# Kernel tuning notes

Hardware: AMD Instinct MI355X
Metric: run time of the kernel (lower is better)

Reference implementation:

```python
import jax, jax.numpy as jnp
import numpy as np

NUM_CLASSES = 12
C_SMOOTH = 5.0  # the `c` constant in compute_weights(distances, 5)


def setup_inputs() -> dict:
    key = jax.random.key(0)
    k1, k2 = jax.random.split(key)
    features = jax.random.normal(k1, (128, 512, 32, 32), dtype=jnp.float32)
    labels = jax.random.randint(k2, (128,), 0, NUM_CLASSES)
    return {"features": features, "labels": labels}


def _prototype_generation(features, labels, num_classes):
    # features: [b, c, h, w]; labels: [b] int
    b = features.shape[0]
    flat = features.reshape(b, -1)  # [b, d], d = c*h*w
    sq = jnp.sum(flat * flat, axis=1)  # [b]
    d2 = sq[:, None] + sq[None, :] - 2.0 * (flat @ flat.T)  # [b, b]
    d2 = jnp.maximum(d2, 0.0)
    # grad-safe sqrt: diagonal (and identical pairs) get dist 0 with grad 0,
    # matching torch.norm's subgradient at 0
    pos = d2 > 0
    dist = jnp.where(pos, jnp.sqrt(jnp.where(pos, d2, 1.0)), 0.0)  # [b, b]
    # sum of distances to same-label samples (includes self, dist 0)
    same = (labels[:, None] == labels[None, :]).astype(flat.dtype)  # [b, b]
    dsum = jnp.sum(dist * same, axis=1)  # [b]
    # compute_weights(distance_sum, 5) = 1 / (sqrt(ds^2 + 25) + 1e-12)
    w = 1.0 / (jnp.sqrt(dsum * dsum + C_SMOOTH * C_SMOOTH) + 1e-12)
    w = w / (jnp.sum(w) + 1e-12)  # normalized sample weights [b]
    # label-grouped weighted scatter-sum -> [num_classes, c, h, w]
    weighted = features * w[:, None, None, None]
    return jax.ops.segment_sum(weighted, labels, num_segments=num_classes)


def reference(features, labels):
    return _prototype_generation(features, labels, NUM_CLASSES)
```

## Files before the change

### kernel.cpp

```cpp
#include <hip/hip_runtime.h>
#include <math.h>

#define D_FEAT 524288
#define NSAMP  128
#define NCLS   12
#define BK     256
#define KPB    2048
#define NB     256
#define D4     131072

typedef __bf16 bf16x8 __attribute__((ext_vector_type(8)));
typedef float  f32x16 __attribute__((ext_vector_type(16)));

__device__ __forceinline__ unsigned pack_bf16(float a, float b) {
  unsigned ua = __float_as_uint(a); ua += 0x7fffu + ((ua >> 16) & 1u);
  unsigned ub = __float_as_uint(b); ub += 0x7fffu + ((ub >> 16) & 1u);
  return (ua >> 16) | (ub & 0xffff0000u);
}

__global__ __launch_bounds__(512, 2) void gram_k(const float* __restrict__ f,
                                                 float* __restrict__ gram,
                                                 float* __restrict__ partial,
                                                 int atomic_mode) {
  __shared__ __align__(16) unsigned char lds[BK * NSAMP * 2];
  const int t    = threadIdx.x;
  const int b    = blockIdx.x;
  const int wave = t >> 6;
  const int lane = t & 63;
  const int sl   = lane & 31;
  const int hi   = lane >> 5;
  const int Ra   = (wave >> 2) * 64;
  const int Ca   = (wave & 3) * 32;
  const int kq   = lane;
  const size_t k0 = (size_t)b * KPB;

  f32x16 acc0, acc1;
#pragma unroll
  for (int i = 0; i < 16; ++i) { acc0[i] = 0.f; acc1[i] = 0.f; }

  const int wg      = kq >> 1;
  const int halfsel = kq & 1;

  float4 pf[16];
#pragma unroll
  for (int i = 0; i < 16; ++i) {
    const int s = i * 8 + wave;
    pf[i] = *(const float4*)(f + (size_t)s * D_FEAT + k0 + kq * 4);
  }
#pragma unroll
  for (int i = 0; i < 16; ++i) {
    const int s = i * 8 + wave;
    uint2 p; p.x = pack_bf16(pf[i].x, pf[i].y); p.y = pack_bf16(pf[i].z, pf[i].w);
    *(uint2*)(lds + (size_t)(wg * NSAMP + (s ^ (wg & 7))) * 16 + halfsel * 8) = p;
  }

  for (int sli = 0; sli < KPB / BK; ++sli) {
    __syncthreads();
    if (sli < KPB / BK - 1) {
      const size_t kb = k0 + (size_t)(sli + 1) * BK;
#pragma unroll
      for (int i = 0; i < 16; ++i) {
        const int s = i * 8 + wave;
        pf[i] = *(const float4*)(f + (size_t)s * D_FEAT + kb + kq * 4);
      }
    }
#pragma unroll
    for (int t16 = 0; t16 < 16; ++t16) {
      const int g = 2 * t16 + hi, gx = g & 7;
      const unsigned char* base = lds + g * (NSAMP * 16);
      bf16x8 a0 = *(const bf16x8*)(base + (((Ra      + sl) ^ gx) << 4));
      bf16x8 a1 = *(const bf16x8*)(base + (((Ra + 32 + sl) ^ gx) << 4));
      bf16x8 b0 = *(const bf16x8*)(base + (((Ca      + sl) ^ gx) << 4));
      acc0 = __builtin_amdgcn_mfma_f32_32x32x16_bf16(a0, b0, acc0, 0, 0, 0);
      acc1 = __builtin_amdgcn_mfma_f32_32x32x16_bf16(a1, b0, acc1, 0, 0, 0);
    }
    __syncthreads();
    if (sli < KPB / BK - 1) {
#pragma unroll
      for (int i = 0; i < 16; ++i) {
        const int s = i * 8 + wave;
        uint2 p; p.x = pack_bf16(pf[i].x, pf[i].y); p.y = pack_bf16(pf[i].z, pf[i].w);
        *(uint2*)(lds + (size_t)(wg * NSAMP + (s ^ (wg & 7))) * 16 + halfsel * 8) = p;
      }
    }
  }

  if (atomic_mode) {
#pragma unroll
    for (int r = 0; r < 16; ++r) {
      const int row0 = Ra + 4 * hi + (r & 3) + 8 * (r >> 2);
      atomicAdd(gram + row0 * NSAMP + Ca + sl, acc0[r]);
      atomicAdd(gram + (row0 + 32) * NSAMP + Ca + sl, acc1[r]);
    }
  } else {
    float* p = partial + (size_t)b * (NSAMP * NSAMP);
#pragma unroll
    for (int r = 0; r < 16; ++r) {
      const int row0 = Ra + 4 * hi + (r & 3) + 8 * (r >> 2);
      p[row0 * NSAMP + Ca + sl]        = acc0[r];
      p[(row0 + 32) * NSAMP + Ca + sl] = acc1[r];
    }
  }
}

__global__ __launch_bounds__(256) void reduce_k(const float* __restrict__ partial,
                                                float* __restrict__ gram) {
  const int idx = blockIdx.x * 256 + threadIdx.x;
  float s = 0.f;
#pragma unroll 8
  for (int b = 0; b < NB; ++b) s += partial[(size_t)b * (NSAMP * NSAMP) + idx];
  gram[idx] = s;
}

__global__ void weights_k(const float* __restrict__ gram, const int* __restrict__ labels,
                          float* __restrict__ w_out, int* __restrict__ order_out,
                          int* __restrict__ off_out) {
  __shared__ float sq[NSAMP];
  __shared__ int   lab[NSAMP];
  __shared__ float wv[NSAMP];
  __shared__ float wsum_s;
  __shared__ int   cnt[NCLS];
  __shared__ int   off[NCLS + 1];
  const int t = threadIdx.x;
  lab[t] = labels[t];
  sq[t]  = gram[t * NSAMP + t];
  if (t < NCLS) cnt[t] = 0;
  __syncthreads();
  const int   myl = lab[t];
  const float st  = sq[t];
  float dsum = 0.f;
  for (int j = 0; j < NSAMP; ++j) {
    if (j != t && lab[j] == myl) {
      float d2 = st + sq[j] - 2.f * gram[t * NSAMP + j];
      if (d2 > 0.f) dsum += sqrtf(d2);
    }
  }
  const float wt = 1.f / (sqrtf(dsum * dsum + 25.f) + 1e-12f);
  wv[t] = wt;
  atomicAdd(&cnt[myl], 1);
  __syncthreads();
  if (t == 0) {
    float s = 0.f;
    for (int j = 0; j < NSAMP; ++j) s += wv[j];
    wsum_s = s;
    off[0] = 0;
    for (int c = 0; c < NCLS; ++c) off[c + 1] = off[c] + cnt[c];
  }
  __syncthreads();
  int rank = 0;
  for (int j = 0; j < t; ++j) rank += (lab[j] == myl) ? 1 : 0;
  const int pos  = off[myl] + rank;
  order_out[pos] = t;
  w_out[pos]     = wt / (wsum_s + 1e-12f);
  if (t <= NCLS) off_out[t] = off[t];
}

__global__ __launch_bounds__(256) void scatter_k(const float* __restrict__ f,
                                                 const float* __restrict__ w,
                                                 const int* __restrict__ order,
                                                 const int* __restrict__ off,
                                                 float* __restrict__ out) {
  __shared__ float w_l[NSAMP];
  __shared__ int   ord_l[NSAMP];
  __shared__ int   off_l[NCLS + 1];
  const int t = threadIdx.x;
  if (t < NSAMP) { w_l[t] = w[t]; ord_l[t] = order[t]; }
  if (t <= NCLS) off_l[t] = off[t];
  __syncthreads();
  const size_t d4 = (size_t)blockIdx.x * 256 + t;
  const float4* f4 = (const float4*)f;
  float4* o4 = (float4*)out;
  for (int c = 0; c < NCLS; ++c) {
    float4 acc = make_float4(0.f, 0.f, 0.f, 0.f);
    const int e = off_l[c + 1];
#pragma unroll 4
    for (int j = off_l[c]; j < e; ++j) {
      const float  wj = w_l[j];
      const float4 v  = f4[(size_t)ord_l[j] * D4 + d4];
      acc.x += wj * v.x; acc.y += wj * v.y; acc.z += wj * v.z; acc.w += wj * v.w;
    }
    o4[(size_t)c * D4 + d4] = acc;
  }
}

extern "C" void kernel_launch(void* const* d_in, const int* in_sizes, int n_in,
                              void* d_out, int out_size, void* d_ws, size_t ws_size,
                              hipStream_t stream) {
  const float* f      = (const float*)d_in[0];
  const int*   labels = (const int*)d_in[1];
  float* out  = (float*)d_out;
  float* ws_f = (float*)d_ws;

  float* gram     = ws_f;
  float* w_sorted = ws_f + 16384;
  int*   order    = (int*)(ws_f + 16384 + 128);
  int*   clsoff   = (int*)(ws_f + 16384 + 256);
  float* partial  = ws_f + 32768;

  const size_t need = (size_t)32768 * 4 + (size_t)NB * NSAMP * NSAMP * 4;
  const int atomic_mode = (ws_size < need) ? 1 : 0;

  if (atomic_mode) hipMemsetAsync(gram, 0, NSAMP * NSAMP * sizeof(float), stream);
  gram_k<<<NB, 512, 0, stream>>>(f, gram, partial, atomic_mode);
  if (!atomic_mode) reduce_k<<<64, 256, 0, stream>>>(partial, gram);
  weights_k<<<1, NSAMP, 0, stream>>>(gram, labels, w_sorted, order, clsoff);
  scatter_k<<<D4 / 256, 256, 0, stream>>>(f, w_sorted, order, clsoff, out);
}
```

Measured before the change: 483.9 us.

## Double-buffer gram LDS tiles, widen reduce grid, stage gram in LDS for weights

The gram kernel now keeps two LDS buffers, so the next bf16 slice is written while the current one is read, and one barrier per iteration is dropped. The partial-sum reduce uses 256 blocks of 64 threads so more CUs pull data. The weights kernel copies the full gram matrix into LDS with 256 threads and sums the weights with a wave shuffle instead of a serial loop. LDS use in gram_k doubles to 128KB, which may limit the intended two blocks per CU.

Measured after the change: 473.0 us. 1.02x faster.

```diff
diff --git a/kernel.cpp b/kernel.cpp
--- a/kernel.cpp
+++ b/kernel.cpp
@@ -22,7 +22,7 @@
                                                  float* __restrict__ gram,
                                                  float* __restrict__ partial,
                                                  int atomic_mode) {
-  __shared__ __align__(16) unsigned char lds[BK * NSAMP * 2];
+  __shared__ __align__(16) unsigned char lds[2 * BK * NSAMP * 2];
   const int t    = threadIdx.x;
   const int b    = blockIdx.x;
   const int wave = t >> 6;
@@ -51,11 +51,13 @@
   for (int i = 0; i < 16; ++i) {
     const int s = i * 8 + wave;
     uint2 p; p.x = pack_bf16(pf[i].x, pf[i].y); p.y = pack_bf16(pf[i].z, pf[i].w);
-    *(uint2*)(lds + (size_t)(wg * NSAMP + (s ^ (wg & 7))) * 16 + halfsel * 8) = p;
+    *(uint2*)(lds + (wg * NSAMP + (s ^ (wg & 7))) * 16 + halfsel * 8) = p;
   }
 
   for (int sli = 0; sli < KPB / BK; ++sli) {
     __syncthreads();
+    const unsigned char* rb = lds + (sli & 1) * (BK * NSAMP * 2);
+    unsigned char*       wb = lds + ((sli + 1) & 1) * (BK * NSAMP * 2);
     if (sli < KPB / BK - 1) {
       const size_t kb = k0 + (size_t)(sli + 1) * BK;
 #pragma unroll
@@ -67,20 +69,19 @@
 #pragma unroll
     for (int t16 = 0; t16 < 16; ++t16) {
       const int g = 2 * t16 + hi, gx = g & 7;
-      const unsigned char* base = lds + g * (NSAMP * 16);
+      const unsigned char* base = rb + g * (NSAMP * 16);
       bf16x8 a0 = *(const bf16x8*)(base + (((Ra      + sl) ^ gx) << 4));
       bf16x8 a1 = *(const bf16x8*)(base + (((Ra + 32 + sl) ^ gx) << 4));
       bf16x8 b0 = *(const bf16x8*)(base + (((Ca      + sl) ^ gx) << 4));
       acc0 = __builtin_amdgcn_mfma_f32_32x32x16_bf16(a0, b0, acc0, 0, 0, 0);
       acc1 = __builtin_amdgcn_mfma_f32_32x32x16_bf16(a1, b0, acc1, 0, 0, 0);
     }
-    __syncthreads();
     if (sli < KPB / BK - 1) {
 #pragma unroll
       for (int i = 0; i < 16; ++i) {
         const int s = i * 8 + wave;
         uint2 p; p.x = pack_bf16(pf[i].x, pf[i].y); p.y = pack_bf16(pf[i].z, pf[i].w);
-        *(uint2*)(lds + (size_t)(wg * NSAMP + (s ^ (wg & 7))) * 16 + halfsel * 8) = p;
+        *(uint2*)(wb + (wg * NSAMP + (s ^ (wg & 7))) * 16 + halfsel * 8) = p;
       }
     }
   }
@@ -103,55 +104,72 @@
   }
 }
 
-__global__ __launch_bounds__(256) void reduce_k(const float* __restrict__ partial,
-                                                float* __restrict__ gram) {
-  const int idx = blockIdx.x * 256 + threadIdx.x;
+__global__ __launch_bounds__(64) void reduce_k(const float* __restrict__ partial,
+                                               float* __restrict__ gram) {
+  const int idx = blockIdx.x * 64 + threadIdx.x;
   float s = 0.f;
-#pragma unroll 8
+#pragma unroll 16
   for (int b = 0; b < NB; ++b) s += partial[(size_t)b * (NSAMP * NSAMP) + idx];
   gram[idx] = s;
 }
 
-__global__ void weights_k(const float* __restrict__ gram, const int* __restrict__ labels,
+__global__ __launch_bounds__(256) void weights_k(const float* __restrict__ gram,
+                          const int* __restrict__ labels,
                           float* __restrict__ w_out, int* __restrict__ order_out,
                           int* __restrict__ off_out) {
-  __shared__ float sq[NSAMP];
+  __shared__ __align__(16) float g[NSAMP * NSAMP];
   __shared__ int   lab[NSAMP];
   __shared__ float wv[NSAMP];
   __shared__ float wsum_s;
   __shared__ int   cnt[NCLS];
   __shared__ int   off[NCLS + 1];
   const int t = threadIdx.x;
-  lab[t] = labels[t];
-  sq[t]  = gram[t * NSAMP + t];
-  if (t < NCLS) cnt[t] = 0;
-  __syncthreads();
-  const int   myl = lab[t];
-  const float st  = sq[t];
-  float dsum = 0.f;
-  for (int j = 0; j < NSAMP; ++j) {
-    if (j != t && lab[j] == myl) {
-      float d2 = st + sq[j] - 2.f * gram[t * NSAMP + j];
-      if (d2 > 0.f) dsum += sqrtf(d2);
-    }
-  }
-  const float wt = 1.f / (sqrtf(dsum * dsum + 25.f) + 1e-12f);
-  wv[t] = wt;
-  atomicAdd(&cnt[myl], 1);
-  __syncthreads();
-  if (t == 0) {
-    float s = 0.f;
-    for (int j = 0; j < NSAMP; ++j) s += wv[j];
-    wsum_s = s;
-    off[0] = 0;
-    for (int c = 0; c < NCLS; ++c) off[c + 1] = off[c] + cnt[c];
-  }
-  __syncthreads();
-  int rank = 0;
-  for (int j = 0; j < t; ++j) rank += (lab[j] == myl) ? 1 : 0;
-  const int pos  = off[myl] + rank;
-  order_out[pos] = t;
-  w_out[pos]     = wt / (wsum_s + 1e-12f);
+
+  {
+    float4* g4 = (float4*)g;
+    const float4* s4 = (const float4*)gram;
+#pragma unroll
+    for (int i = 0; i < 16; ++i) g4[i * 256 + t] = s4[i * 256 + t];
+  }
+  if (t < NSAMP) lab[t] = labels[t];
+  if (t < NCLS)  cnt[t] = 0;
+  __syncthreads();
+
+  if (t < NSAMP) {
+    const int   myl = lab[t];
+    const float st  = g[t * NSAMP + t];
+    float dsum = 0.f;
+    for (int j = 0; j < NSAMP; ++j) {
+      if (j != t && lab[j] == myl) {
+        float d2 = st + g[j * NSAMP + j] - 2.f * g[t * NSAMP + j];
+        if (d2 > 0.f) dsum += sqrtf(d2);
+      }
+    }
+    wv[t] = 1.f / (sqrtf(dsum * dsum + 25.f) + 1e-12f);
+    atomicAdd(&cnt[myl], 1);
+  }
+  __syncthreads();
+
+  if (t < 64) {
+    float s = wv[t] + wv[t + 64];
+#pragma unroll
+    for (int o = 32; o > 0; o >>= 1) s += __shfl_down(s, o);
+    if (t == 0) {
+      wsum_s = s;
+      off[0] = 0;
+      for (int c = 0; c < NCLS; ++c) off[c + 1] = off[c] + cnt[c];
+    }
+  }
+  __syncthreads();
+
+  if (t < NSAMP) {
+    const int myl = lab[t];
+    int rank = 0;
+    for (int j = 0; j < t; ++j) rank += (lab[j] == myl) ? 1 : 0;
+    const int pos  = off[myl] + rank;
+    order_out[pos] = t;
+    w_out[pos]     = wv[t] / (wsum_s + 1e-12f);
+  }
   if (t <= NCLS) off_out[t] = off[t];
 }
 
@@ -202,7 +220,7 @@
 
   if (atomic_mode) hipMemsetAsync(gram, 0, NSAMP * NSAMP * sizeof(float), stream);
   gram_k<<<NB, 512, 0, stream>>>(f, gram, partial, atomic_mode);
-  if (!atomic_mode) reduce_k<<<64, 256, 0, stream>>>(partial, gram);
-  weights_k<<<1, NSAMP, 0, stream>>>(gram, labels, w_sorted, order, clsoff);
+  if (!atomic_mode) reduce_k<<<256, 64, 0, stream>>>(partial, gram);
+  weights_k<<<1, 256, 0, stream>>>(gram, labels, w_sorted, order, clsoff);
   scatter_k<<<D4 / 256, 256, 0, stream>>>(f, w_sorted, order, clsoff, out);
 }
```
